# Optimization experiments

Measured on AMD Instinct MI355X. Metric: run time of the kernel, lower is better.

Reference implementation:

```python
import jax, jax.numpy as jnp
import numpy as np
from math import factorial

MAXL = 5
TAUS = [8, 8, 8, 8, 8, 8]
OUT_TAUS = [8, 8, 8, 8, 8, 8]
BM_EPS = 1e-5
BATCH = 1024


def _cg_coeff(l1, l2, l, m1, m2, m):
    # Standard Clebsch-Gordan coefficient <l1 m1 l2 m2 | l m> (Racah formula).
    if m1 + m2 != m:
        return 0.0
    f = factorial
    pre = ((2 * l + 1) * f(l + l1 - l2) * f(l - l1 + l2) * f(l1 + l2 - l) / f(l1 + l2 + l + 1)) ** 0.5
    pre *= (f(l + m) * f(l - m) * f(l1 - m1) * f(l1 + m1) * f(l2 - m2) * f(l2 + m2)) ** 0.5
    s = 0.0
    for k in range(0, l1 + l2 - l + 1):
        ds = [k, l1 + l2 - l - k, l1 - m1 - k, l2 + m2 - k, l - l2 + m1 + k, l - l1 - m2 + k]
        if min(ds) < 0:
            continue
        d = 1.0
        for v in ds:
            d *= f(v)
        s += (-1.0) ** k / d
    return pre * s


def _cg_block(l1, l2, l):
    C = np.zeros((2 * l + 1, 2 * l1 + 1, 2 * l2 + 1), dtype=np.float32)
    for m in range(-l, l + 1):
        for m1 in range(-l1, l1 + 1):
            m2 = m - m1
            if -l2 <= m2 <= l2:
                C[m + l, m1 + l1, m2 + l2] = _cg_coeff(l1, l2, l, m1, m2, m)
    return C


# Triple enumeration order matches cal_middle_taus (l1 outer, l2, then l).
TRIPLES = []
for _l1 in range(MAXL + 1):
    for _l2 in range(_l1 + 1):
        for _l in range(_l1 - _l2, min(_l1 + _l2, MAXL) + 1):
            TRIPLES.append((_l1, _l2, _l))
CG_BLOCKS = [jnp.asarray(_cg_block(*t)) for t in TRIPLES]

MIDDLE_TAUS = np.zeros(MAXL + 1, dtype=np.int64)
for (_l1, _l2, _l) in TRIPLES:
    MIDDLE_TAUS[_l] += TAUS[_l1] * TAUS[_l2]
IN_LEN = int(sum(TAUS[l] * (2 * l + 1) for l in range(MAXL + 1)))    # 288
OUT_LEN = int(sum(OUT_TAUS[l] * (2 * l + 1) for l in range(MAXL + 1)))  # 288
WLEN = int(sum(OUT_TAUS[l] * int(MIDDLE_TAUS[l]) for l in range(MAXL + 1)))  # 35328
STD_LEN = int(MIDDLE_TAUS.sum())  # 4416


def _forward(activations, weights, moving_std):
    B = activations.shape[0]
    act = activations[..., 0] + 1j * activations[..., 1]  # [B, IN_LEN] complex64
    # split into per-degree blocks F[l]: [B, tau_l, 2l+1]
    F = []
    st = 0
    for l in range(MAXL + 1):
        n = TAUS[l] * (2 * l + 1)
        F.append(act[:, st:st + n].reshape(B, TAUS[l], 2 * l + 1))
        st += n
    # CG tensor product: one fragment per (l1,l2,l) triple, grouped by output degree l
    mids = [[] for _ in range(MAXL + 1)]
    for (l1, l2, l), C in zip(TRIPLES, CG_BLOCKS):
        frag = jnp.einsum('mac,bta,bsc->btsm', C.astype(act.dtype), F[l1], F[l2])
        mids[l].append(frag.reshape(B, TAUS[l1] * TAUS[l2], 2 * l + 1))
    # per-fragment batchnorm (divide by running std) + per-degree complex mixing
    outs = []
    so = 0
    wo = 0
    for l in range(MAXL + 1):
        mid = jnp.concatenate(mids[l], axis=1)  # [B, middle_taus[l], 2l+1]
        nt = int(MIDDLE_TAUS[l])
        std = moving_std[so:so + nt]
        so += nt
        mid = mid / (std + BM_EPS)[None, :, None]
        nw = OUT_TAUS[l] * nt
        wl = weights[wo:wo + nw]
        wo += nw
        Wc = (wl[:, 0] + 1j * wl[:, 1]).reshape(OUT_TAUS[l], nt)
        out = jnp.einsum('ot,btm->bom', Wc, mid)  # [B, out_taus[l], 2l+1]
        outs.append(out.reshape(B, OUT_TAUS[l] * (2 * l + 1)))
    oc = jnp.concatenate(outs, axis=1)  # [B, OUT_LEN] complex
    return jnp.stack([oc.real, oc.imag], axis=-1)  # [B, OUT_LEN, 2]


def setup_inputs() -> dict:
    key = jax.random.key(0)
    k1, k2, k3 = jax.random.split(key, 3)
    activations = jax.random.normal(k1, (BATCH, IN_LEN, 2), dtype=jnp.float32)
    weights = 0.05 * jax.random.uniform(k2, (WLEN, 2), dtype=jnp.float32)
    moving_std = 0.1 + 0.9 * jax.random.uniform(k3, (STD_LEN,), dtype=jnp.float32)
    return {"activations": activations, "weights": weights, "moving_std": moving_std}


def reference(activations, weights, moving_std):
    return _forward(activations, weights, moving_std)
```

## Files before the change

kernel.cpp:

```cpp
#include <hip/hip_runtime.h>
#include <hip/hip_bf16.h>
#include <utility>


constexpr int NTRIP = 69;
constexpr int NL    = 6;
constexpr int BATCH = 1024;
constexpr int ROW   = 288;
constexpr int MID_LDS = 2880;
constexpr int MAXIT = 64;
constexpr int MAXCH = 4;

struct Meta {
    int tl1[NTRIP], tl2[NTRIP], tll[NTRIP];
    int tf1[NTRIP], tf2[NTRIP];
    int ttloc[NTRIP];
    int trip_of_l[NL][16];
    int ntrips[NL];
    int mid_tau[NL], std_off[NL], w_off[NL], f_l[NL];
    int nch[NL];
    int ch_start[NL][MAXCH], ch_cnt[NL][MAXCH];
    int nit[NL];
    int it_slot[NL][MAXIT], it_m0[NL][MAXIT], it_m1[NL][MAXIT];
    int it_wave[NL][MAXIT], it_ch[NL][MAXIT];
};

constexpr int win_lo(int l1, int l2, int l, int mi) {
    int v = mi - l + l1 - l2; return v < 0 ? 0 : v;
}
constexpr int win_hi(int l1, int l2, int l, int mi) {
    int v = mi - l + l1 + l2; return v > 2 * l1 ? 2 * l1 : v;
}

constexpr Meta build_meta() {
    Meta m{};
    int fl[NL] = {};
    {
        int acc = 0;
        for (int l = 0; l < NL; l++) { fl[l] = acc; m.f_l[l] = acc; acc += 8 * (2 * l + 1); }
    }
    int idx = 0;
    for (int l1 = 0; l1 <= 5; l1++)
        for (int l2 = 0; l2 <= l1; l2++) {
            int lmax = (l1 + l2 < 5) ? (l1 + l2) : 5;
            for (int l = l1 - l2; l <= lmax; l++) {
                m.tl1[idx] = l1; m.tl2[idx] = l2; m.tll[idx] = l;
                m.tf1[idx] = fl[l1]; m.tf2[idx] = fl[l2];
                m.ttloc[idx] = 64 * m.ntrips[l];
                m.trip_of_l[l][m.ntrips[l]] = idx;
                m.ntrips[l]++;
                idx++;
            }
        }
    int so = 0, wo = 0;
    for (int l = 0; l < NL; l++) {
        m.mid_tau[l] = 64 * m.ntrips[l];
        m.std_off[l] = so; so += m.mid_tau[l];
        m.w_off[l]   = wo; wo += 8 * m.mid_tau[l];
    }
    for (int l = 0; l < NL; l++) {
        const int TW = 2 * l + 1;
        const int maxslot = MID_LDS / (64 * TW);
        const int ntl = m.ntrips[l];
        const int nch = (ntl + maxslot - 1) / maxslot;
        m.nch[l] = nch;
        if (nch > MAXCH) return Meta{};
        int done = 0;
        for (int c = 0; c < nch; c++) {
            int cnt = (ntl - done + (nch - c) - 1) / (nch - c);
            m.ch_start[l][c] = done; m.ch_cnt[l][c] = cnt; done += cnt;
        }
        const int npmax = (l <= 2) ? 1 : (l <= 4 ? 2 : 4);
        int nit = 0;
        for (int c = 0; c < nch; c++) {
            const int it_first = nit;
            for (int si = m.ch_start[l][c]; si < m.ch_start[l][c] + m.ch_cnt[l][c]; si++) {
                int trip = m.trip_of_l[l][si];
                int l1 = m.tl1[trip], l2 = m.tl2[trip];
                int wm[16] = {}; int tot = 0;
                for (int mi = 0; mi < TW; mi++) {
                    wm[mi] = win_hi(l1, l2, l, mi) - win_lo(l1, l2, l, mi) + 1;
                    tot += wm[mi];
                }
                int np = npmax;
                if (np > TW) np = TW;
                int mcur = 0, acc2 = 0;
                for (int p = 0; p < np; p++) {
                    int target = (tot * (p + 1)) / np;
                    int m0 = mcur;
                    while (mcur < TW - (np - 1 - p) && (acc2 < target || mcur == m0)) {
                        acc2 += wm[mcur]; mcur++;
                    }
                    if (nit >= MAXIT) return Meta{};
                    m.it_slot[l][nit] = si;
                    m.it_m0[l][nit] = m0;
                    m.it_m1[l][nit] = mcur - 1;
                    m.it_ch[l][nit] = c;
                    nit++;
                }
            }
            int cost[MAXIT] = {}; bool asg[MAXIT] = {};
            for (int i = it_first; i < nit; i++) {
                int trip = m.trip_of_l[l][m.it_slot[l][i]];
                int l1 = m.tl1[trip], l2 = m.tl2[trip];
                int tc = 0;
                for (int mi = m.it_m0[l][i]; mi <= m.it_m1[l][i]; mi++)
                    tc += win_hi(l1, l2, l, mi) - win_lo(l1, l2, l, mi) + 1;
                cost[i] = tc * 6 + (2 * l1 + 2 * l2 + 2) * 2;
            }
            int load[4] = {};
            for (int k = it_first; k < nit; k++) {
                int best = -1, bc = -1;
                for (int i = it_first; i < nit; i++)
                    if (!asg[i] && cost[i] > bc) { bc = cost[i]; best = i; }
                asg[best] = true;
                int wsel = 0;
                for (int w2 = 1; w2 < 4; w2++) if (load[w2] < load[wsel]) wsel = w2;
                m.it_wave[l][best] = wsel;
                load[wsel] += bc;
            }
        }
        m.nit[l] = nit;
    }
    return m;
}

constexpr Meta MT = build_meta();
constexpr int WLEN = 35328;
static_assert(MT.w_off[5] + 8 * MT.mid_tau[5] == WLEN, "wlen (meta poisoned?)");
static_assert(MT.std_off[5] + MT.mid_tau[5] == 4416, "stdlen");
static_assert(MT.nch[3] <= MAXCH && MT.nch[4] <= MAXCH && MT.nch[5] <= MAXCH, "nch");

constexpr double cfact(int n) {
    double r = 1.0;
    for (int i = 2; i <= n; i++) r *= (double)i;
    return r;
}
constexpr double csqrt(double x) {
    double g = x > 1.0 ? x : 1.0;
    for (int i = 0; i < 100; i++) g = 0.5 * (g + x / g);
    return g;
}
constexpr float cg_coeff(int l1, int l2, int l, int m1, int m2, int m) {
    if (m1 + m2 != m) return 0.0f;
    double pre = csqrt((double)(2 * l + 1) * cfact(l + l1 - l2) * cfact(l - l1 + l2) *
                       cfact(l1 + l2 - l) / cfact(l1 + l2 + l + 1));
    pre *= csqrt(cfact(l + m) * cfact(l - m) * cfact(l1 - m1) * cfact(l1 + m1) *
                 cfact(l2 - m2) * cfact(l2 + m2));
    double s = 0.0;
    for (int k = 0; k <= l1 + l2 - l; k++) {
        int d0 = k, d1 = l1 + l2 - l - k, d2 = l1 - m1 - k;
        int d3 = l2 + m2 - k, d4 = l - l2 + m1 + k, d5 = l - l1 - m2 + k;
        if (d0 < 0 || d1 < 0 || d2 < 0 || d3 < 0 || d4 < 0 || d5 < 0) continue;
        double den = cfact(d0) * cfact(d1) * cfact(d2) * cfact(d3) * cfact(d4) * cfact(d5);
        s += ((k & 1) ? -1.0 : 1.0) / den;
    }
    return (float)(pre * s);
}

constexpr int rng_alo(int l1, int l2, int l, int m0, int m1) {
    int r = 2 * l1;
    for (int mi = m0; mi <= m1; mi++) { int v = win_lo(l1, l2, l, mi); if (v < r) r = v; }
    return r;
}
constexpr int rng_ahi(int l1, int l2, int l, int m0, int m1) {
    int r = 0;
    for (int mi = m0; mi <= m1; mi++) { int v = win_hi(l1, l2, l, mi); if (v > r) r = v; }
    return r;
}
constexpr int rng_clo(int l1, int l2, int l, int m0, int m1) {
    int r = 2 * l2;
    for (int mi = m0; mi <= m1; mi++) {
        int v = (mi - l) + l1 + l2 - win_hi(l1, l2, l, mi); if (v < r) r = v;
    }
    return r;
}
constexpr int rng_chi(int l1, int l2, int l, int m0, int m1) {
    int r = 0;
    for (int mi = m0; mi <= m1; mi++) {
        int v = (mi - l) + l1 + l2 - win_lo(l1, l2, l, mi); if (v > r) r = v;
    }
    return r;
}

template <int... Is, class F>
__device__ __forceinline__ void static_for_impl(std::integer_sequence<int, Is...>, F&& f) {
    (f(std::integral_constant<int, Is>{}), ...);
}
template <int N, class F>
__device__ __forceinline__ void static_for(F&& f) {
    static_for_impl(std::make_integer_sequence<int, N>{}, (F&&)f);
}

template <int L>
__device__ __forceinline__ void process_l(int b, int tid,
                                          const float2* __restrict__ F,
                                          float2* __restrict__ mid,
                                          const float2* __restrict__ wts,
                                          const float* __restrict__ stdv,
                                          float2* __restrict__ out) {
    constexpr int TW  = 2 * L + 1;
    constexpr int NCH = MT.nch[L];
    constexpr int NT  = MT.mid_tau[L];

    const int wid  = tid >> 6;
    const int lane = tid & 63;
    const int t = lane >> 3, s = lane & 7;

    float2 acc0[TW], acc1[TW];
#pragma unroll
    for (int i = 0; i < TW; i++) { acc0[i] = make_float2(0.f, 0.f); acc1[i] = make_float2(0.f, 0.f); }

    static_for<NCH>([&](auto CHc) {
        constexpr int CH  = decltype(CHc)::value;
        constexpr int S0  = MT.ch_start[L][CH];
        constexpr int CNT = MT.ch_cnt[L][CH];
        constexpr int CT  = CNT * 64;
        static_assert(CT * TW <= MID_LDS, "chunk fits");

        __syncthreads();

        static_for<MT.nit[L]>([&](auto ITc) {
            constexpr int IT = decltype(ITc)::value;
            if constexpr (MT.it_ch[L][IT] == CH) {
                constexpr int SI   = MT.it_slot[L][IT];
                constexpr int TRIP = MT.trip_of_l[L][SI];
                constexpr int L1   = MT.tl1[TRIP];
                constexpr int L2v  = MT.tl2[TRIP];
                constexpr int N1   = 2 * L1 + 1, N2 = 2 * L2v + 1;
                constexpr int M0   = MT.it_m0[L][IT], M1 = MT.it_m1[L][IT];
                constexpr int ALO  = rng_alo(L1, L2v, L, M0, M1);
                constexpr int AHI  = rng_ahi(L1, L2v, L, M0, M1);
                constexpr int CLO  = rng_clo(L1, L2v, L, M0, M1);
                constexpr int CHI_ = rng_chi(L1, L2v, L, M0, M1);
                if (MT.it_wave[L][IT] == wid) {
                    const float2* F1 = F + MT.tf1[TRIP] + t * N1;
                    const float2* F2 = F + MT.tf2[TRIP] + s * N2;
                    float2 f1[AHI - ALO + 1], f2[CHI_ - CLO + 1];
#pragma unroll
                    for (int i = 0; i <= AHI - ALO; i++) f1[i] = F1[ALO + i];
#pragma unroll
                    for (int i = 0; i <= CHI_ - CLO; i++) f2[i] = F2[CLO + i];
                    const int Tloc = (MT.ttloc[TRIP] - S0 * 64) + lane;
                    static_for<M1 - M0 + 1>([&](auto MIc) {
                        constexpr int MI   = M0 + decltype(MIc)::value;
                        constexpr int BASE = MI - L;
                        constexpr int LO   = win_lo(L1, L2v, L, MI);
                        constexpr int HI   = win_hi(L1, L2v, L, MI);
                        float re = 0.f, im = 0.f;
                        static_for<HI - LO + 1>([&](auto Kc) {
                            constexpr int AI = LO + decltype(Kc)::value;
                            constexpr int CI = BASE + L1 + L2v - AI;
                            constexpr float cv = cg_coeff(L1, L2v, L, AI - L1, CI - L2v, BASE);
                            if constexpr (cv != 0.0f) {
                                const float2 a = f1[AI - ALO], c2 = f2[CI - CLO];
                                re = fmaf(cv, fmaf(-a.y, c2.y, a.x * c2.x), re);
                                im = fmaf(cv, fmaf(a.y, c2.x, a.x * c2.y), im);
                            }
                        });
                        mid[MI * CT + Tloc] = make_float2(re, im);
                    });
                }
            }
        });
        __syncthreads();

        const float2* W0 = wts + MT.w_off[L] + wid * NT + S0 * 64;
        const float2* W1 = wts + MT.w_off[L] + (wid + 4) * NT + S0 * 64;
        const float*  Sb = stdv + MT.std_off[L] + S0 * 64;
        for (int T = lane * 2; T < CT; T += 128) {
            const float4 w0r = *reinterpret_cast<const float4*>(W0 + T);
            const float4 w1r = *reinterpret_cast<const float4*>(W1 + T);
            const float2 sd  = *reinterpret_cast<const float2*>(Sb + T);
            const float i0 = __builtin_amdgcn_rcpf(sd.x + 1e-5f);
            const float i1 = __builtin_amdgcn_rcpf(sd.y + 1e-5f);
            const float4 w0 = make_float4(w0r.x * i0, w0r.y * i0, w0r.z * i1, w0r.w * i1);
            const float4 w1 = make_float4(w1r.x * i0, w1r.y * i0, w1r.z * i1, w1r.w * i1);
#pragma unroll
            for (int mi = 0; mi < TW; mi++) {
                const float4 mv = *reinterpret_cast<const float4*>(mid + mi * CT + T);
                acc0[mi].x = fmaf(w0.x, mv.x, fmaf(-w0.y, mv.y,
                              fmaf(w0.z, mv.z, fmaf(-w0.w, mv.w, acc0[mi].x))));
                acc0[mi].y = fmaf(w0.x, mv.y, fmaf(w0.y, mv.x,
                              fmaf(w0.z, mv.w, fmaf(w0.w, mv.z, acc0[mi].y))));
                acc1[mi].x = fmaf(w1.x, mv.x, fmaf(-w1.y, mv.y,
                              fmaf(w1.z, mv.z, fmaf(-w1.w, mv.w, acc1[mi].x))));
                acc1[mi].y = fmaf(w1.x, mv.y, fmaf(w1.y, mv.x,
                              fmaf(w1.z, mv.w, fmaf(w1.w, mv.z, acc1[mi].y))));
            }
        }
    });

    const bool lo = (lane < 32);
    float2 red[TW];
#pragma unroll
    for (int mi = 0; mi < TW; mi++) {
        float gx = lo ? acc1[mi].x : acc0[mi].x;
        float gy = lo ? acc1[mi].y : acc0[mi].y;
        float rx = (lo ? acc0[mi].x : acc1[mi].x) + __shfl_xor(gx, 32, 64);
        float ry = (lo ? acc0[mi].y : acc1[mi].y) + __shfl_xor(gy, 32, 64);
#pragma unroll
        for (int off = 16; off >= 1; off >>= 1) {
            rx += __shfl_xor(rx, off, 64);
            ry += __shfl_xor(ry, off, 64);
        }
        red[mi] = make_float2(rx, ry);
    }
    if (lane == 0 || lane == 32) {
        const int o = wid + (lo ? 0 : 4);
        float2* orow = out + (size_t)b * ROW + MT.f_l[L] + o * TW;
#pragma unroll
        for (int mi = 0; mi < TW; mi++) orow[mi] = red[mi];
    }
}

__global__ __launch_bounds__(256, 4) void fup_main(const float2* __restrict__ act,
                                                   const float2* __restrict__ wts,
                                                   const float* __restrict__ stdv,
                                                   float2* __restrict__ out) {
    __shared__ float2 F[ROW];
    __shared__ __align__(16) float2 mid[MID_LDS];
    const int b = blockIdx.x;
    const int tid = threadIdx.x;
    const float2* arow = act + (size_t)b * ROW;
    for (int i = tid; i < ROW; i += 256) F[i] = arow[i];
    process_l<0>(b, tid, F, mid, wts, stdv, out);
    process_l<1>(b, tid, F, mid, wts, stdv, out);
    process_l<2>(b, tid, F, mid, wts, stdv, out);
    process_l<3>(b, tid, F, mid, wts, stdv, out);
    process_l<4>(b, tid, F, mid, wts, stdv, out);
    process_l<5>(b, tid, F, mid, wts, stdv, out);
}

extern "C" void kernel_launch(void* const* d_in, const int* in_sizes, int n_in,
                              void* d_out, int out_size, void* d_ws, size_t ws_size,
                              hipStream_t stream) {
    const float2* act  = (const float2*)d_in[0];
    const float2* wts  = (const float2*)d_in[1];
    const float*  stdv = (const float*)d_in[2];
    float2* out = (float2*)d_out;

    hipLaunchKernelGGL(fup_main, dim3(BATCH), dim3(256), 0, stream,
                       act, wts, stdv, out);
}
```

Baseline: 119.8 us.

## Use packed FP32 FMAs for complex math and enlarge LDS mid buffer

Rewrites the CG product and the weight-contraction inner loops to use two-wide vector FMAs, so the real and imaginary parts are updated together, with pre-swapped operands for the cross terms. The LDS mid buffer grows from 2880 to 4224 entries, which cuts the number of chunks (and their barriers) for higher degrees. The split of work items for l=5 drops from 4 to 2 per triple. The larger LDS footprint may lower occupancy at 4 blocks per CU, and the extra swapped copies raise register use.

```diff
diff --git a/kernel.cpp b/kernel.cpp
--- a/kernel.cpp
+++ b/kernel.cpp
@@ -2,14 +2,16 @@
 #include <hip/hip_bf16.h>
 #include <utility>
 
+
+typedef float v2f __attribute__((ext_vector_type(2)));
 
 constexpr int NTRIP = 69;
 constexpr int NL    = 6;
 constexpr int BATCH = 1024;
 constexpr int ROW   = 288;
-constexpr int MID_LDS = 2880;
+constexpr int MID_LDS = 4224;
 constexpr int MAXIT = 64;
-constexpr int MAXCH = 4;
+constexpr int MAXCH = 3;
 
 struct Meta {
     int tl1[NTRIP], tl2[NTRIP], tll[NTRIP];
@@ -70,7 +72,7 @@
             int cnt = (ntl - done + (nch - c) - 1) / (nch - c);
             m.ch_start[l][c] = done; m.ch_cnt[l][c] = cnt; done += cnt;
         }
-        const int npmax = (l <= 2) ? 1 : (l <= 4 ? 2 : 4);
+        const int npmax = (l <= 2) ? 1 : 2;
         int nit = 0;
         for (int c = 0; c < nch; c++) {
             const int it_first = nit;
@@ -106,7 +108,7 @@
                 int tc = 0;
                 for (int mi = m.it_m0[l][i]; mi <= m.it_m1[l][i]; mi++)
                     tc += win_hi(l1, l2, l, mi) - win_lo(l1, l2, l, mi) + 1;
-                cost[i] = tc * 6 + (2 * l1 + 2 * l2 + 2) * 2;
+                cost[i] = tc * 3 + (2 * l1 + 2 * l2 + 2) * 2;
             }
             int load[4] = {};
             for (int k = it_first; k < nit; k++) {
@@ -129,7 +131,7 @@
 constexpr int WLEN = 35328;
 static_assert(MT.w_off[5] + 8 * MT.mid_tau[5] == WLEN, "wlen (meta poisoned?)");
 static_assert(MT.std_off[5] + MT.mid_tau[5] == 4416, "stdlen");
-static_assert(MT.nch[3] <= MAXCH && MT.nch[4] <= MAXCH && MT.nch[5] <= MAXCH, "nch");
+static_assert(MT.nch[4] <= MAXCH && MT.nch[5] <= MAXCH, "nch");
 
 constexpr double cfact(int n) {
     double r = 1.0;
@@ -192,10 +194,15 @@
     static_for_impl(std::make_integer_sequence<int, N>{}, (F&&)f);
 }
 
+__device__ __forceinline__ v2f pk_fma(v2f a, v2f b, v2f c) {
+    return __builtin_elementwise_fma(a, b, c);
+}
+__device__ __forceinline__ v2f splat(float x) { v2f r; r.x = x; r.y = x; return r; }
+
 template <int L>
 __device__ __forceinline__ void process_l(int b, int tid,
-                                          const float2* __restrict__ F,
-                                          float2* __restrict__ mid,
+                                          const v2f* __restrict__ F,
+                                          v2f* __restrict__ mid,
                                           const float2* __restrict__ wts,
                                           const float* __restrict__ stdv,
                                           float2* __restrict__ out) {
@@ -207,9 +214,9 @@
     const int lane = tid & 63;
     const int t = lane >> 3, s = lane & 7;
 
-    float2 acc0[TW], acc1[TW];
-#pragma unroll
-    for (int i = 0; i < TW; i++) { acc0[i] = make_float2(0.f, 0.f); acc1[i] = make_float2(0.f, 0.f); }
+    v2f acc0[TW], acc1[TW];
+#pragma unroll
+    for (int i = 0; i < TW; i++) { acc0[i] = splat(0.f); acc1[i] = splat(0.f); }
 
     static_for<NCH>([&](auto CHc) {
         constexpr int CH  = decltype(CHc)::value;
@@ -234,31 +241,37 @@
                 constexpr int CLO  = rng_clo(L1, L2v, L, M0, M1);
                 constexpr int CHI_ = rng_chi(L1, L2v, L, M0, M1);
                 if (MT.it_wave[L][IT] == wid) {
-                    const float2* F1 = F + MT.tf1[TRIP] + t * N1;
-                    const float2* F2 = F + MT.tf2[TRIP] + s * N2;
-                    float2 f1[AHI - ALO + 1], f2[CHI_ - CLO + 1];
+                    const v2f* F1 = F + MT.tf1[TRIP] + t * N1;
+                    const v2f* F2 = F + MT.tf2[TRIP] + s * N2;
+                    v2f f1[AHI - ALO + 1], f2[CHI_ - CLO + 1], f2s[CHI_ - CLO + 1];
 #pragma unroll
                     for (int i = 0; i <= AHI - ALO; i++) f1[i] = F1[ALO + i];
 #pragma unroll
-                    for (int i = 0; i <= CHI_ - CLO; i++) f2[i] = F2[CLO + i];
+                    for (int i = 0; i <= CHI_ - CLO; i++) {
+                        v2f c = F2[CLO + i];
+                        f2[i] = c;
+                        v2f cs; cs.x = -c.y; cs.y = c.x;
+                        f2s[i] = cs;
+                    }
                     const int Tloc = (MT.ttloc[TRIP] - S0 * 64) + lane;
                     static_for<M1 - M0 + 1>([&](auto MIc) {
                         constexpr int MI   = M0 + decltype(MIc)::value;
                         constexpr int BASE = MI - L;
                         constexpr int LO   = win_lo(L1, L2v, L, MI);
                         constexpr int HI   = win_hi(L1, L2v, L, MI);
-                        float re = 0.f, im = 0.f;
+                        v2f accv = splat(0.f);
                         static_for<HI - LO + 1>([&](auto Kc) {
                             constexpr int AI = LO + decltype(Kc)::value;
                             constexpr int CI = BASE + L1 + L2v - AI;
                             constexpr float cv = cg_coeff(L1, L2v, L, AI - L1, CI - L2v, BASE);
                             if constexpr (cv != 0.0f) {
-                                const float2 a = f1[AI - ALO], c2 = f2[CI - CLO];
-                                re = fmaf(cv, fmaf(-a.y, c2.y, a.x * c2.x), re);
-                                im = fmaf(cv, fmaf(a.y, c2.x, a.x * c2.y), im);
+                                const v2f a = f1[AI - ALO];
+                                v2f inner = pk_fma(splat(a.x), f2[CI - CLO],
+                                                   splat(a.y) * f2s[CI - CLO]);
+                                accv = pk_fma(splat(cv), inner, accv);
                             }
                         });
-                        mid[MI * CT + Tloc] = make_float2(re, im);
+                        mid[MI * CT + Tloc] = accv;
                     });
                 }
             }
@@ -274,19 +287,25 @@
             const float2 sd  = *reinterpret_cast<const float2*>(Sb + T);
             const float i0 = __builtin_amdgcn_rcpf(sd.x + 1e-5f);
             const float i1 = __builtin_amdgcn_rcpf(sd.y + 1e-5f);
-            const float4 w0 = make_float4(w0r.x * i0, w0r.y * i0, w0r.z * i1, w0r.w * i1);
-            const float4 w1 = make_float4(w1r.x * i0, w1r.y * i0, w1r.z * i1, w1r.w * i1);
+            const v2f wx0a = splat(w0r.x * i0), wy0a = splat(w0r.y * i0);
+            const v2f wx0b = splat(w0r.z * i1), wy0b = splat(w0r.w * i1);
+            const v2f wx1a = splat(w1r.x * i0), wy1a = splat(w1r.y * i0);
+            const v2f wx1b = splat(w1r.z * i1), wy1b = splat(w1r.w * i1);
 #pragma unroll
             for (int mi = 0; mi < TW; mi++) {
                 const float4 mv = *reinterpret_cast<const float4*>(mid + mi * CT + T);
-                acc0[mi].x = fmaf(w0.x, mv.x, fmaf(-w0.y, mv.y,
-                              fmaf(w0.z, mv.z, fmaf(-w0.w, mv.w, acc0[mi].x))));
-                acc0[mi].y = fmaf(w0.x, mv.y, fmaf(w0.y, mv.x,
-                              fmaf(w0.z, mv.w, fmaf(w0.w, mv.z, acc0[mi].y))));
-                acc1[mi].x = fmaf(w1.x, mv.x, fmaf(-w1.y, mv.y,
-                              fmaf(w1.z, mv.z, fmaf(-w1.w, mv.w, acc1[mi].x))));
-                acc1[mi].y = fmaf(w1.x, mv.y, fmaf(w1.y, mv.x,
-                              fmaf(w1.z, mv.w, fmaf(w1.w, mv.z, acc1[mi].y))));
+                v2f m0; m0.x = mv.x; m0.y = mv.y;
+                v2f m1; m1.x = mv.z; m1.y = mv.w;
+                v2f m0s; m0s.x = -mv.y; m0s.y = mv.x;
+                v2f m1s; m1s.x = -mv.w; m1s.y = mv.z;
+                acc0[mi] = pk_fma(wx0a, m0, acc0[mi]);
+                acc0[mi] = pk_fma(wy0a, m0s, acc0[mi]);
+                acc0[mi] = pk_fma(wx0b, m1, acc0[mi]);
+                acc0[mi] = pk_fma(wy0b, m1s, acc0[mi]);
+                acc1[mi] = pk_fma(wx1a, m0, acc1[mi]);
+                acc1[mi] = pk_fma(wy1a, m0s, acc1[mi]);
+                acc1[mi] = pk_fma(wx1b, m1, acc1[mi]);
+                acc1[mi] = pk_fma(wy1b, m1s, acc1[mi]);
             }
         }
     });
@@ -318,12 +337,16 @@
                                                    const float2* __restrict__ wts,
                                                    const float* __restrict__ stdv,
                                                    float2* __restrict__ out) {
-    __shared__ float2 F[ROW];
-    __shared__ __align__(16) float2 mid[MID_LDS];
+    __shared__ v2f F[ROW];
+    __shared__ __align__(16) v2f mid[MID_LDS];
     const int b = blockIdx.x;
     const int tid = threadIdx.x;
     const float2* arow = act + (size_t)b * ROW;
-    for (int i = tid; i < ROW; i += 256) F[i] = arow[i];
+    for (int i = tid; i < ROW; i += 256) {
+        float2 v = arow[i];
+        v2f f; f.x = v.x; f.y = v.y;
+        F[i] = f;
+    }
     process_l<0>(b, tid, F, mid, wts, stdv, out);
     process_l<1>(b, tid, F, mid, wts, stdv, out);
     process_l<2>(b, tid, F, mid, wts, stdv, out);
```

Result: slower. 127.1 us (+6.0%).
